# Optimization experiments

Hardware: AMD Instinct MI355X
Metric: run time of the kernel (lower is better)

## Reference

```python
import jax, jax.numpy as jnp
import numpy as np

B, LAT, NF, IMG, NC = 16, 512, 32, 128, 12
WT_FIN, WT_FOUT = NF * 64, NF                 # wave_bias_transform dyna 1x1 conv
C2C_FIN, C2C_FH, C2C_FOUT = NF * 4, NF * 2, NF * 2  # cell_to_cell dyna residual block (gated -> fout=2*NF)


def _inorm(x, eps=1e-5):
    # F.instance_norm (no affine): per-sample, per-channel over H,W
    m = x.mean(axis=(2, 3), keepdims=True)
    v = ((x - m) ** 2).mean(axis=(2, 3), keepdims=True)
    return (x - m) * jax.lax.rsqrt(v + eps)


def _sobel_kernels(nf):
    # SinSobel(nf, 3, 1): sin gradient profile x cos smoothing profile, 2 directions (c_factor=2)
    xs = jnp.array([-1.0, 0.0, 1.0], dtype=jnp.float32)
    g = jnp.sin(xs * (np.pi / 2))
    s = jnp.cos(xs * (np.pi / 2))
    ky = jnp.outer(g, s)
    kx = jnp.outer(s, g)
    k = jnp.stack([ky, kx])[:, None]          # [2,1,3,3]
    return jnp.tile(k, (nf, 1, 1, 1))         # [2*nf,1,3,3] depthwise


def _hyper(lat, w1, b1, w2, b2):
    h = jax.nn.relu(lat @ w1 + b1)
    return h @ w2 + b2


def _dyn_params(p, fin, fout, off):
    w = p[:, off:off + fin * fout].reshape(-1, fout, fin) / np.sqrt(fin)
    b = p[:, off + fin * fout: off + fin * fout + fout]
    return w, b, off + fin * fout + fout


def _econv(x, w, b):
    # per-sample dynamic 1x1 conv: x [B,I,H,W], w [B,O,I], b [B,O]
    return jnp.einsum('bihw,boi->bohw', x, w) + b[:, :, None, None]


def setup_inputs():
    key = jax.random.key(0)
    ks = jax.random.split(key, 8)
    sc = 0.02
    P = (C2C_FIN * C2C_FH + C2C_FH) + (C2C_FH * C2C_FH + C2C_FH) + \
        (C2C_FH * C2C_FOUT + C2C_FOUT) + (C2C_FIN * C2C_FOUT + C2C_FOUT)
    WP = WT_FIN * WT_FOUT + WT_FOUT
    return {
        'lat': jax.random.normal(ks[0], (B, LAT), jnp.float32),
        'leak_factor': jnp.asarray(0.1, jnp.float32),
        'wave_bias': jax.random.normal(ks[1], (1, WT_FIN, IMG, IMG), jnp.float32),
        'wt_w1': jax.random.normal(ks[2], (LAT, LAT), jnp.float32) * sc,
        'wt_b1': jnp.zeros((LAT,), jnp.float32),
        'wt_w2': jax.random.normal(ks[3], (LAT, WP), jnp.float32) * sc,
        'wt_b2': jnp.zeros((WP,), jnp.float32),
        'c2c_w1': jax.random.normal(ks[4], (LAT, 2 * LAT), jnp.float32) * sc,
        'c2c_b1': jnp.zeros((2 * LAT,), jnp.float32),
        'c2c_w2': jax.random.normal(ks[5], (2 * LAT, P), jnp.float32) * sc,
        'c2c_b2': jnp.zeros((P,), jnp.float32),
        'out_w': jax.random.normal(ks[6], (3, NF), jnp.float32) / np.sqrt(NF),
        'out_b': jnp.zeros((3,), jnp.float32),
    }


def reference(lat, leak_factor, wave_bias, wt_w1, wt_b1, wt_w2, wt_b2,
              c2c_w1, c2c_b1, c2c_w2, c2c_b2, out_w, out_b):
    b = lat.shape[0]
    # wave bias: per-sample dynamic 1x1 conv -> exp(i*x) -> cat(real, imag) -> instance norm
    pw = _hyper(lat, wt_w1, wt_b1, wt_w2, wt_b2)
    ww, wbb, _ = _dyn_params(pw, WT_FIN, WT_FOUT, 0)
    wb_flat = _econv(jnp.broadcast_to(wave_bias, (b,) + wave_bias.shape[1:]), ww, wbb)
    wave = _inorm(jnp.concatenate([jnp.cos(wb_flat), jnp.sin(wb_flat)], axis=1))  # [B,2*NF,H,W]
    leak = jnp.clip(leak_factor, 1e-3, 1e3)
    # cell_to_cell hypernetwork-generated residual-block weights (shared across calls)
    p = _hyper(lat, c2c_w1, c2c_b1, c2c_w2, c2c_b2)
    w_in, b_in, o = _dyn_params(p, C2C_FIN, C2C_FH, 0)
    w_mid, b_mid, o = _dyn_params(p, C2C_FH, C2C_FH, o)
    w_out, b_out, o = _dyn_params(p, C2C_FH, C2C_FOUT, o)
    w_sk, b_sk, o = _dyn_params(p, C2C_FIN, C2C_FOUT, o)
    kern = _sobel_kernels(NF)

    def step(out, _):
        g = _inorm(jax.lax.conv_general_dilated(
            out, kern, (1, 1), 'SAME', feature_group_count=NF,
            dimension_numbers=('NCHW', 'OIHW', 'NCHW')))
        xin = jnp.concatenate([g, wave], axis=1)             # [B,4*NF,H,W]
        h = jax.nn.leaky_relu(_econv(xin, w_in, b_in), 0.2)
        h = jax.nn.leaky_relu(_econv(h, w_mid, b_mid), 0.2)
        y = _econv(h, w_out, b_out) + _econv(xin, w_sk, b_sk)  # [B,2*NF,H,W]
        out_new = y[:, :NF] * jax.nn.sigmoid(y[:, NF:])        # gated
        nxt = out + leak * out_new
        return nxt, nxt

    out0 = jnp.zeros((b, NF, IMG, IMG), jnp.float32)
    out, embs = jax.lax.scan(step, out0, None, length=NC)
    out_embs = jnp.concatenate([out0[None], embs], axis=0)     # [NC+1,B,NF,H,W]
    out_raw = jnp.einsum('bihw,oi->bohw', out, out_w) + out_b[None, :, None, None]
    return jnp.clip(out_raw, -1.0, 1.0), out_embs, out_raw
```

## Files before the change

### kernel.cpp

```cpp
#include <hip/hip_runtime.h>
#include <hip/hip_bf16.h>
#include <stdint.h>


typedef __attribute__((ext_vector_type(8))) short s8v;
typedef __attribute__((ext_vector_type(4))) float f4v;

__device__ __forceinline__ uint16_t f2b(float f) {
    uint32_t x = __builtin_bit_cast(uint32_t, f);
    uint32_t r = (x + 0x7fffu + ((x >> 16) & 1u)) >> 16;
    return (uint16_t)r;
}

__device__ __forceinline__ float blockReduceSum(float v, float* scratch) {
    #pragma unroll
    for (int o = 32; o > 0; o >>= 1) v += __shfl_down(v, o, 64);
    int w = threadIdx.x >> 6;
    if ((threadIdx.x & 63) == 0) scratch[w] = v;
    __syncthreads();
    float r = scratch[0] + scratch[1] + scratch[2] + scratch[3];
    __syncthreads();
    return r;
}

__global__ __launch_bounds__(256) void k_hyper1(const float* __restrict__ lat,
        const float* __restrict__ w1a, const float* __restrict__ b1a,
        const float* __restrict__ w1b, const float* __restrict__ b1b,
        float* __restrict__ hwtT, float* __restrict__ hc2cT) {
    int b = blockIdx.y;
    int j = blockIdx.x * 256 + threadIdx.x;
    __shared__ float lats[512];
    for (int k = threadIdx.x; k < 512; k += 256) lats[k] = lat[b * 512 + k];
    __syncthreads();
    if (j < 512) {
        float acc = b1a[j];
        #pragma unroll 4
        for (int k = 0; k < 512; k++) acc += lats[k] * w1a[k * 512 + j];
        hwtT[j * 16 + b] = fmaxf(acc, 0.f);
    } else {
        int jj = j - 512;
        float acc = b1b[jj];
        #pragma unroll 4
        for (int k = 0; k < 512; k++) acc += lats[k] * w1b[k * 1024 + jj];
        hc2cT[jj * 16 + b] = fmaxf(acc, 0.f);
    }
}

__global__ __launch_bounds__(256) void k_hyper2(const float* __restrict__ hT,
        const float* __restrict__ w2, const float* __restrict__ b2v,
        float* __restrict__ outp, int K, int N) {
    extern __shared__ float hs[];
    for (int i = threadIdx.x; i < K * 16; i += 256) hs[i] = hT[i];
    __syncthreads();
    int col = blockIdx.x * 256 + threadIdx.x;
    if (col >= N) return;
    float acc[16];
    float bias = b2v[col];
    #pragma unroll
    for (int b = 0; b < 16; b++) acc[b] = bias;
    #pragma unroll 4
    for (int k = 0; k < K; k++) {
        float wv = w2[(size_t)k * N + col];
        const f4v* h4 = (const f4v*)(hs + k * 16);
        f4v h0 = h4[0], h1 = h4[1], h2 = h4[2], h3 = h4[3];
        acc[0]  += h0[0] * wv; acc[1]  += h0[1] * wv; acc[2]  += h0[2] * wv; acc[3]  += h0[3] * wv;
        acc[4]  += h1[0] * wv; acc[5]  += h1[1] * wv; acc[6]  += h1[2] * wv; acc[7]  += h1[3] * wv;
        acc[8]  += h2[0] * wv; acc[9]  += h2[1] * wv; acc[10] += h2[2] * wv; acc[11] += h2[3] * wv;
        acc[12] += h3[0] * wv; acc[13] += h3[1] * wv; acc[14] += h3[2] * wv; acc[15] += h3[3] * wv;
    }
    #pragma unroll
    for (int b = 0; b < 16; b++) outp[(size_t)b * N + col] = acc[b];
}

__global__ __launch_bounds__(256) void k_prepw(const float* __restrict__ pw, const float* __restrict__ pc,
        uint16_t* __restrict__ ww, uint16_t* __restrict__ wc) {
    int tid = blockIdx.x * 256 + threadIdx.x;
    const float s128 = 0.08838834764831845f;
    const float s64  = 0.125f;
    const float s2048 = 0.02209708691207961f;
    if (tid < 16 * 65536) {
        int b = tid >> 16, r = tid & 65535;
        ww[tid] = f2b(pw[(size_t)b * 65568 + r] * s2048);
    } else {
        int t = tid - 16 * 65536;
        int b = t / 24576, r = t % 24576;
        int src; float sc;
        if (r < 8192)       { src = r;                   sc = s128; }
        else if (r < 12288) { src = 8256  + (r - 8192);  sc = s64; }
        else if (r < 16384) { src = 12416 + (r - 12288); sc = s64; }
        else                { src = 16576 + (r - 16384); sc = s128; }
        wc[(size_t)b * 24576 + r] = f2b(pc[(size_t)b * 24832 + src] * sc);
    }
}

__global__ __launch_bounds__(256) void k_transpose(const float* __restrict__ wb, uint16_t* __restrict__ wbt) {
    __shared__ uint16_t tile[64][66];
    int p0 = blockIdx.x * 64, i0 = blockIdx.y * 64;
    int lane = threadIdx.x & 63, grp = threadIdx.x >> 6;
    #pragma unroll
    for (int r = 0; r < 16; r++) {
        int i = grp * 16 + r;
        tile[i][lane] = f2b(wb[(size_t)(i0 + i) * 16384 + p0 + lane]);
    }
    __syncthreads();
    #pragma unroll
    for (int r = 0; r < 16; r++) {
        int p = grp * 16 + r;
        wbt[(size_t)(p0 + p) * 2048 + i0 + lane] = tile[lane][p];
    }
}

__global__ __launch_bounds__(256) void k_wavegemm(const uint16_t* __restrict__ ww,
        const uint16_t* __restrict__ wbt, const float* __restrict__ pw, float* __restrict__ wb) {
    int nt = blockIdx.x;
    int mt = blockIdx.y;
    int w = threadIdx.x >> 6, L = threadIdx.x & 63;
    int l15 = L & 15, quad = L >> 4;
    int pxbase = nt * 256 + w * 64;
    f4v acc[4][4];
    #pragma unroll
    for (int t = 0; t < 4; t++) {
        int m = mt * 64 + t * 16 + quad * 4;
        int b = m >> 5, o = m & 31;
        f4v bv = *(const f4v*)(pw + (size_t)b * 65568 + 65536 + o);
        #pragma unroll
        for (int j = 0; j < 4; j++) acc[t][j] = bv;
    }
    for (int kk = 0; kk < 64; kk++) {
        s8v a[4], x[4];
        #pragma unroll
        for (int t = 0; t < 4; t++) {
            int m = mt * 64 + t * 16 + l15;
            a[t] = *(const s8v*)(ww + (size_t)m * 2048 + kk * 32 + quad * 8);
        }
        #pragma unroll
        for (int j = 0; j < 4; j++) {
            int p = pxbase + j * 16 + l15;
            x[j] = *(const s8v*)(wbt + (size_t)p * 2048 + kk * 32 + quad * 8);
        }
        #pragma unroll
        for (int t = 0; t < 4; t++)
            #pragma unroll
            for (int j = 0; j < 4; j++)
                acc[t][j] = __builtin_amdgcn_mfma_f32_16x16x32_bf16(a[t], x[j], acc[t][j], 0, 0, 0);
    }
    #pragma unroll
    for (int t = 0; t < 4; t++)
        #pragma unroll
        for (int j = 0; j < 4; j++)
            #pragma unroll
            for (int r = 0; r < 4; r++) {
                int row = mt * 64 + t * 16 + quad * 4 + r;
                int p = pxbase + j * 16 + l15;
                wb[(size_t)row * 16384 + p] = acc[t][j][r];
            }
}

__global__ __launch_bounds__(256) void k_wavestats(const float* __restrict__ wb, float* __restrict__ stats) {
    __shared__ float scratch[4];
    int c = blockIdx.x, b = blockIdx.y;
    const float* src = wb + (size_t)(b * 32 + (c & 31)) * 16384;
    bool isc = c < 32;
    float s = 0.f;
    for (int p = threadIdx.x; p < 16384; p += 256) {
        float x = src[p];
        s += isc ? __cosf(x) : __sinf(x);
    }
    float m = blockReduceSum(s, scratch) * (1.f / 16384.f);
    float s2 = 0.f;
    for (int p = threadIdx.x; p < 16384; p += 256) {
        float x = src[p];
        float v = (isc ? __cosf(x) : __sinf(x)) - m;
        s2 += v * v;
    }
    float tv = blockReduceSum(s2, scratch);
    if (threadIdx.x == 0) {
        stats[(b * 64 + c) * 2 + 0] = m;
        stats[(b * 64 + c) * 2 + 1] = rsqrtf(tv * (1.f / 16384.f) + 1e-5f);
    }
}

__global__ __launch_bounds__(256) void k_wavewrite(const float* __restrict__ wb,
        const float* __restrict__ stats, uint16_t* __restrict__ xin) {
    __shared__ uint16_t tl[256][66];
    int b = blockIdx.y, p0 = blockIdx.x * 256;
    int t = threadIdx.x;
    for (int c = 0; c < 64; c++) {
        int row = b * 32 + (c & 31);
        float m  = stats[(b * 64 + c) * 2 + 0];
        float rs = stats[(b * 64 + c) * 2 + 1];
        float x = wb[(size_t)row * 16384 + p0 + t];
        float v = (c < 32) ? __cosf(x) : __sinf(x);
        tl[t][c] = f2b((v - m) * rs);
    }
    __syncthreads();
    uint16_t* dst = xin + ((size_t)(b * 16384 + p0 + t) * 128 + 64);
    const uint32_t* s32 = (const uint32_t*)&tl[t][0];
    #pragma unroll
    for (int c8 = 0; c8 < 64; c8 += 8) {
        uint4 v;
        v.x = s32[c8 / 2 + 0]; v.y = s32[c8 / 2 + 1];
        v.z = s32[c8 / 2 + 2]; v.w = s32[c8 / 2 + 3];
        *(uint4*)(dst + c8) = v;
    }
}

__global__ __launch_bounds__(256) void k_gstats(const float* __restrict__ outs, float* __restrict__ stats) {
    __shared__ float scratch[4];
    int ic = blockIdx.x, b = blockIdx.y;
    const float* src = outs + (size_t)(b * 32 + ic) * 16384;
    float sy = 0.f, sy2 = 0.f, sx = 0.f, sx2 = 0.f;
    for (int p = threadIdx.x; p < 16384; p += 256) {
        int y = p >> 7, x = p & 127;
        float up = (y > 0)   ? src[p - 128] : 0.f;
        float dn = (y < 127) ? src[p + 128] : 0.f;
        float lf = (x > 0)   ? src[p - 1]   : 0.f;
        float rt = (x < 127) ? src[p + 1]   : 0.f;
        float vy = dn - up, vx = rt - lf;
        sy += vy; sy2 += vy * vy; sx += vx; sx2 += vx * vx;
    }
    float SY  = blockReduceSum(sy,  scratch);
    float SY2 = blockReduceSum(sy2, scratch);
    float SX  = blockReduceSum(sx,  scratch);
    float SX2 = blockReduceSum(sx2, scratch);
    if (threadIdx.x == 0) {
        float my = SY * (1.f / 16384.f);
        float vy = fmaxf(SY2 * (1.f / 16384.f) - my * my, 0.f);
        float mx = SX * (1.f / 16384.f);
        float vx = fmaxf(SX2 * (1.f / 16384.f) - mx * mx, 0.f);
        stats[(b * 64 + 2 * ic) * 2 + 0] = my;
        stats[(b * 64 + 2 * ic) * 2 + 1] = rsqrtf(vy + 1e-5f);
        stats[(b * 64 + 2 * ic + 1) * 2 + 0] = mx;
        stats[(b * 64 + 2 * ic + 1) * 2 + 1] = rsqrtf(vx + 1e-5f);
    }
}

__global__ __launch_bounds__(256) void k_gwrite(const float* __restrict__ outs,
        const float* __restrict__ stats, uint16_t* __restrict__ xin) {
    __shared__ uint16_t tl[256][66];
    int b = blockIdx.y, p0 = blockIdx.x * 256;
    int t = threadIdx.x;
    int p = p0 + t;
    int y = p >> 7, x = p & 127;
    for (int ic = 0; ic < 32; ic++) {
        const float* src = outs + (size_t)(b * 32 + ic) * 16384;
        float up = (y > 0)   ? src[p - 128] : 0.f;
        float dn = (y < 127) ? src[p + 128] : 0.f;
        float lf = (x > 0)   ? src[p - 1]   : 0.f;
        float rt = (x < 127) ? src[p + 1]   : 0.f;
        int o = 2 * ic;
        float m0 = stats[(b * 64 + o) * 2], r0 = stats[(b * 64 + o) * 2 + 1];
        float m1 = stats[(b * 64 + o + 1) * 2], r1 = stats[(b * 64 + o + 1) * 2 + 1];
        tl[t][o]     = f2b((dn - up - m0) * r0);
        tl[t][o + 1] = f2b((rt - lf - m1) * r1);
    }
    __syncthreads();
    uint16_t* dst = xin + (size_t)(b * 16384 + p) * 128;
    const uint32_t* s32 = (const uint32_t*)&tl[t][0];
    #pragma unroll
    for (int c8 = 0; c8 < 64; c8 += 8) {
        uint4 v;
        v.x = s32[c8 / 2 + 0]; v.y = s32[c8 / 2 + 1];
        v.z = s32[c8 / 2 + 2]; v.w = s32[c8 / 2 + 3];
        *(uint4*)(dst + c8) = v;
    }
}

__global__ __launch_bounds__(256) void k_conv(const uint16_t* __restrict__ wc,
        const uint16_t* __restrict__ xin, const float* __restrict__ pc,
        float* __restrict__ outs, float* __restrict__ embs, const float* __restrict__ leakp) {
    __shared__ uint16_t Hs[256][72];
    int b = blockIdx.y, p0 = blockIdx.x * 256;
    int w = threadIdx.x >> 6, L = threadIdx.x & 63;
    int l15 = L & 15, quad = L >> 4;
    const uint16_t* wcb = wc + (size_t)b * 24576;
    const float* pcb = pc + (size_t)b * 24832;
    size_t xbase = ((size_t)b * 16384 + p0 + w * 64) * 128;

    f4v acc[4][4];
    #pragma unroll
    for (int t = 0; t < 4; t++) {
        f4v bv = *(const f4v*)(pcb + 8192 + t * 16 + quad * 4);
        #pragma unroll
        for (int j = 0; j < 4; j++) acc[t][j] = bv;
    }
    #pragma unroll
    for (int kk = 0; kk < 4; kk++) {
        s8v a[4], x[4];
        #pragma unroll
        for (int t = 0; t < 4; t++)
            a[t] = *(const s8v*)(wcb + (size_t)(t * 16 + l15) * 128 + kk * 32 + quad * 8);
        #pragma unroll
        for (int j = 0; j < 4; j++)
            x[j] = *(const s8v*)(xin + xbase + (size_t)(j * 16 + l15) * 128 + kk * 32 + quad * 8);
        #pragma unroll
        for (int t = 0; t < 4; t++)
            #pragma unroll
            for (int j = 0; j < 4; j++)
                acc[t][j] = __builtin_amdgcn_mfma_f32_16x16x32_bf16(a[t], x[j], acc[t][j], 0, 0, 0);
    }
    #pragma unroll
    for (int t = 0; t < 4; t++)
        #pragma unroll
        for (int j = 0; j < 4; j++) {
            uint16_t pk[4];
            #pragma unroll
            for (int r = 0; r < 4; r++) {
                float v = acc[t][j][r];
                pk[r] = f2b(v > 0.f ? v : 0.2f * v);
            }
            int px = w * 64 + j * 16 + l15;
            int ch = t * 16 + quad * 4;
            uint2 u; u.x = (uint32_t)pk[0] | ((uint32_t)pk[1] << 16);
            u.y = (uint32_t)pk[2] | ((uint32_t)pk[3] << 16);
            *(uint2*)&Hs[px][ch] = u;
        }
    __syncthreads();

    f4v acc2[4][4];
    #pragma unroll
    for (int t = 0; t < 4; t++) {
        f4v bv = *(const f4v*)(pcb + 12352 + t * 16 + quad * 4);
        #pragma unroll
        for (int j = 0; j < 4; j++) acc2[t][j] = bv;
    }
    #pragma unroll
    for (int kk = 0; kk < 2; kk++) {
        s8v a[4], h[4];
        #pragma unroll
        for (int t = 0; t < 4; t++)
            a[t] = *(const s8v*)(wcb + 8192 + (size_t)(t * 16 + l15) * 64 + kk * 32 + quad * 8);
        #pragma unroll
        for (int j = 0; j < 4; j++) {
            int px = w * 64 + j * 16 + l15;
            h[j] = *(const s8v*)&Hs[px][kk * 32 + quad * 8];
        }
        #pragma unroll
        for (int t = 0; t < 4; t++)
            #pragma unroll
            for (int j = 0; j < 4; j++)
                acc2[t][j] = __builtin_amdgcn_mfma_f32_16x16x32_bf16(a[t], h[j], acc2[t][j], 0, 0, 0);
    }
    __syncthreads();
    #pragma unroll
    for (int t = 0; t < 4; t++)
        #pragma unroll
        for (int j = 0; j < 4; j++) {
            uint16_t pk[4];
            #pragma unroll
            for (int r = 0; r < 4; r++) {
                float v = acc2[t][j][r];
                pk[r] = f2b(v > 0.f ? v : 0.2f * v);
            }
            int px = w * 64 + j * 16 + l15;
            int ch = t * 16 + quad * 4;
            uint2 u; u.x = (uint32_t)pk[0] | ((uint32_t)pk[1] << 16);
            u.y = (uint32_t)pk[2] | ((uint32_t)pk[3] << 16);
            *(uint2*)&Hs[px][ch] = u;
        }
    __syncthreads();

    f4v acc3[4][4];
    #pragma unroll
    for (int t = 0; t < 4; t++) {
        f4v b1 = *(const f4v*)(pcb + 16512 + t * 16 + quad * 4);
        f4v b2 = *(const f4v*)(pcb + 24768 + t * 16 + quad * 4);
        f4v bv = b1 + b2;
        #pragma unroll
        for (int j = 0; j < 4; j++) acc3[t][j] = bv;
    }
    #pragma unroll
    for (int kk = 0; kk < 2; kk++) {
        s8v a[4], h[4];
        #pragma unroll
        for (int t = 0; t < 4; t++)
            a[t] = *(const s8v*)(wcb + 12288 + (size_t)(t * 16 + l15) * 64 + kk * 32 + quad * 8);
        #pragma unroll
        for (int j = 0; j < 4; j++) {
            int px = w * 64 + j * 16 + l15;
            h[j] = *(const s8v*)&Hs[px][kk * 32 + quad * 8];
        }
        #pragma unroll
        for (int t = 0; t < 4; t++)
            #pragma unroll
            for (int j = 0; j < 4; j++)
                acc3[t][j] = __builtin_amdgcn_mfma_f32_16x16x32_bf16(a[t], h[j], acc3[t][j], 0, 0, 0);
    }
    #pragma unroll
    for (int kk = 0; kk < 4; kk++) {
        s8v a[4], x[4];
        #pragma unroll
        for (int t = 0; t < 4; t++)
            a[t] = *(const s8v*)(wcb + 16384 + (size_t)(t * 16 + l15) * 128 + kk * 32 + quad * 8);
        #pragma unroll
        for (int j = 0; j < 4; j++)
            x[j] = *(const s8v*)(xin + xbase + (size_t)(j * 16 + l15) * 128 + kk * 32 + quad * 8);
        #pragma unroll
        for (int t = 0; t < 4; t++)
            #pragma unroll
            for (int j = 0; j < 4; j++)
                acc3[t][j] = __builtin_amdgcn_mfma_f32_16x16x32_bf16(a[t], x[j], acc3[t][j], 0, 0, 0);
    }

    float leak = leakp[0];
    leak = fminf(fmaxf(leak, 0.001f), 1000.f);
    #pragma unroll
    for (int t = 0; t < 2; t++)
        #pragma unroll
        for (int j = 0; j < 4; j++) {
            int px = p0 + w * 64 + j * 16 + l15;
            #pragma unroll
            for (int r = 0; r < 4; r++) {
                int ch = t * 16 + quad * 4 + r;
                float y1 = acc3[t][j][r];
                float y2 = acc3[t + 2][j][r];
                float on = y1 / (1.f + __expf(-y2));
                size_t idx = (size_t)(b * 32 + ch) * 16384 + px;
                float nx = outs[idx] + leak * on;
                outs[idx] = nx;
                embs[idx] = nx;
            }
        }
}

__global__ __launch_bounds__(256) void k_final(const float* __restrict__ outs,
        const float* __restrict__ ow, const float* __restrict__ ob,
        float* __restrict__ dclip, float* __restrict__ draw) {
    __shared__ float ws[3][32];
    __shared__ float obs[3];
    int b = blockIdx.y, p0 = blockIdx.x * 256;
    int t = threadIdx.x;
    if (t < 96) ws[t / 32][t % 32] = ow[t];
    if (t < 3) obs[t] = ob[t];
    __syncthreads();
    int p = p0 + t;
    float a0 = obs[0], a1 = obs[1], a2 = obs[2];
    #pragma unroll 4
    for (int c = 0; c < 32; c++) {
        float v = outs[(size_t)(b * 32 + c) * 16384 + p];
        a0 += v * ws[0][c]; a1 += v * ws[1][c]; a2 += v * ws[2][c];
    }
    float raw[3] = {a0, a1, a2};
    #pragma unroll
    for (int oc = 0; oc < 3; oc++) {
        size_t idx = (size_t)(b * 3 + oc) * 16384 + p;
        draw[idx] = raw[oc];
        dclip[idx] = fminf(fmaxf(raw[oc], -1.f), 1.f);
    }
}

extern "C" void kernel_launch(void* const* d_in, const int* in_sizes, int n_in,
                              void* d_out, int out_size, void* d_ws, size_t ws_size,
                              hipStream_t stream) {
    const float* lat   = (const float*)d_in[0];
    const float* leakp = (const float*)d_in[1];
    const float* wbias = (const float*)d_in[2];
    const float* wtw1  = (const float*)d_in[3];
    const float* wtb1  = (const float*)d_in[4];
    const float* wtw2  = (const float*)d_in[5];
    const float* wtb2  = (const float*)d_in[6];
    const float* cw1   = (const float*)d_in[7];
    const float* cb1   = (const float*)d_in[8];
    const float* cw2   = (const float*)d_in[9];
    const float* cb2   = (const float*)d_in[10];
    const float* outw  = (const float*)d_in[11];
    const float* outb  = (const float*)d_in[12];
    float* out_f = (float*)d_out;

    char* ws = (char*)d_ws;
    float*    hwtT  = (float*)(ws + 0);
    float*    hc2cT = (float*)(ws + 32768);
    float*    pw    = (float*)(ws + 98304);
    float*    pc    = (float*)(ws + 4294656);
    uint16_t* ww    = (uint16_t*)(ws + 5883904);
    uint16_t* wc    = (uint16_t*)(ws + 7981056);
    float*    statw = (float*)(ws + 8767488);
    float*    statg = (float*)(ws + 8775680);
    float*    wb    = (float*)(ws + 8783872);
    uint16_t* wbt   = (uint16_t*)(ws + 42338304);
    uint16_t* xin   = (uint16_t*)(ws + 109447168);
    float*    outs  = (float*)(ws + 176556032);

    hipMemsetAsync(outs, 0, 33554432, stream);
    hipMemsetAsync(out_f + 786432, 0, 33554432, stream);

    k_hyper1<<<dim3(6, 16), 256, 0, stream>>>(lat, wtw1, wtb1, cw1, cb1, hwtT, hc2cT);
    k_hyper2<<<dim3(257), 256, 32768, stream>>>(hwtT, wtw2, wtb2, pw, 512, 65568);
    k_hyper2<<<dim3(97), 256, 65536, stream>>>(hc2cT, cw2, cb2, pc, 1024, 24832);
    k_prepw<<<dim3(5632), 256, 0, stream>>>(pw, pc, ww, wc);
    k_transpose<<<dim3(256, 32), 256, 0, stream>>>(wbias, wbt);
    k_wavegemm<<<dim3(64, 8), 256, 0, stream>>>(ww, wbt, pw, wb);
    k_wavestats<<<dim3(64, 16), 256, 0, stream>>>(wb, statw);
    k_wavewrite<<<dim3(64, 16), 256, 0, stream>>>(wb, statw, xin);

    for (int it = 0; it < 12; ++it) {
        k_gstats<<<dim3(32, 16), 256, 0, stream>>>(outs, statg);
        k_gwrite<<<dim3(64, 16), 256, 0, stream>>>(outs, statg, xin);
        k_conv<<<dim3(64, 16), 256, 0, stream>>>(wc, xin, pc, outs,
                out_f + 786432 + (size_t)(it + 1) * 8388608, leakp);
    }
    k_final<<<dim3(64, 16), 256, 0, stream>>>(outs, outw, outb, out_f, out_f + 109838336);
}
```

Measured before the change: 2.466 ms.

## Ping-pong state through embedding slots, fuse sin/cos stats, remap wave GEMM blocks

The recurrent state is no longer kept in a separate buffer. Each step reads the previous embedding slot and writes the next one, which removes a read-modify-write and a duplicate store per step, and the first gstats launch is skipped because it would read an all-zero state. The wave stats kernel now computes the cos and sin statistics in one pass over half as many blocks, and wavewrite computes sincos once per element with the stats cached in shared memory. The wave GEMM gets an XCD-aware block-to-tile mapping plus a 2x unroll, and the conv kernel computes the skip GEMM together with the first GEMM so the x loads are shared, at the cost of higher register pressure from holding two accumulator sets.

```diff
diff --git a/kernel.cpp b/kernel.cpp
--- a/kernel.cpp
+++ b/kernel.cpp
@@ -112,8 +112,10 @@
 
 __global__ __launch_bounds__(256) void k_wavegemm(const uint16_t* __restrict__ ww,
         const uint16_t* __restrict__ wbt, const float* __restrict__ pw, float* __restrict__ wb) {
-    int nt = blockIdx.x;
-    int mt = blockIdx.y;
+    int id = blockIdx.x;
+    int xcd = id & 7, slot = id >> 3;
+    int nt = xcd * 8 + (slot >> 3);
+    int mt = slot & 7;
     int w = threadIdx.x >> 6, L = threadIdx.x & 63;
     int l15 = L & 15, quad = L >> 4;
     int pxbase = nt * 256 + w * 64;
@@ -126,6 +128,7 @@
         #pragma unroll
         for (int j = 0; j < 4; j++) acc[t][j] = bv;
     }
+    #pragma unroll 2
     for (int kk = 0; kk < 64; kk++) {
         s8v a[4], x[4];
         #pragma unroll
@@ -159,39 +162,43 @@
 __global__ __launch_bounds__(256) void k_wavestats(const float* __restrict__ wb, float* __restrict__ stats) {
     __shared__ float scratch[4];
     int c = blockIdx.x, b = blockIdx.y;
-    const float* src = wb + (size_t)(b * 32 + (c & 31)) * 16384;
-    bool isc = c < 32;
-    float s = 0.f;
+    const float* src = wb + (size_t)(b * 32 + c) * 16384;
+    float sc = 0.f, sc2 = 0.f, ss = 0.f, ss2 = 0.f;
     for (int p = threadIdx.x; p < 16384; p += 256) {
         float x = src[p];
-        s += isc ? __cosf(x) : __sinf(x);
-    }
-    float m = blockReduceSum(s, scratch) * (1.f / 16384.f);
-    float s2 = 0.f;
-    for (int p = threadIdx.x; p < 16384; p += 256) {
-        float x = src[p];
-        float v = (isc ? __cosf(x) : __sinf(x)) - m;
-        s2 += v * v;
-    }
-    float tv = blockReduceSum(s2, scratch);
+        float cv = __cosf(x), sv = __sinf(x);
+        sc += cv; sc2 += cv * cv; ss += sv; ss2 += sv * sv;
+    }
+    float SC  = blockReduceSum(sc,  scratch);
+    float SC2 = blockReduceSum(sc2, scratch);
+    float SS  = blockReduceSum(ss,  scratch);
+    float SS2 = blockReduceSum(ss2, scratch);
     if (threadIdx.x == 0) {
-        stats[(b * 64 + c) * 2 + 0] = m;
-        stats[(b * 64 + c) * 2 + 1] = rsqrtf(tv * (1.f / 16384.f) + 1e-5f);
+        float mc = SC * (1.f / 16384.f);
+        float vc = fmaxf(SC2 * (1.f / 16384.f) - mc * mc, 0.f);
+        float ms = SS * (1.f / 16384.f);
+        float vs = fmaxf(SS2 * (1.f / 16384.f) - ms * ms, 0.f);
+        stats[(b * 64 + c) * 2 + 0] = mc;
+        stats[(b * 64 + c) * 2 + 1] = rsqrtf(vc + 1e-5f);
+        stats[(b * 64 + 32 + c) * 2 + 0] = ms;
+        stats[(b * 64 + 32 + c) * 2 + 1] = rsqrtf(vs + 1e-5f);
     }
 }
 
 __global__ __launch_bounds__(256) void k_wavewrite(const float* __restrict__ wb,
         const float* __restrict__ stats, uint16_t* __restrict__ xin) {
     __shared__ uint16_t tl[256][66];
+    __shared__ float sst[128];
     int b = blockIdx.y, p0 = blockIdx.x * 256;
     int t = threadIdx.x;
-    for (int c = 0; c < 64; c++) {
-        int row = b * 32 + (c & 31);
-        float m  = stats[(b * 64 + c) * 2 + 0];
-        float rs = stats[(b * 64 + c) * 2 + 1];
+    if (t < 128) sst[t] = stats[b * 128 + t];
+    __syncthreads();
+    for (int c = 0; c < 32; c++) {
+        int row = b * 32 + c;
         float x = wb[(size_t)row * 16384 + p0 + t];
-        float v = (c < 32) ? __cosf(x) : __sinf(x);
-        tl[t][c] = f2b((v - m) * rs);
+        float cv = __cosf(x), sv = __sinf(x);
+        tl[t][c]      = f2b((cv - sst[2 * c]) * sst[2 * c + 1]);
+        tl[t][c + 32] = f2b((sv - sst[64 + 2 * c]) * sst[64 + 2 * c + 1]);
     }
     __syncthreads();
     uint16_t* dst = xin + ((size_t)(b * 16384 + p0 + t) * 128 + 64);
@@ -205,10 +212,10 @@
     }
 }
 
-__global__ __launch_bounds__(256) void k_gstats(const float* __restrict__ outs, float* __restrict__ stats) {
+__global__ __launch_bounds__(256) void k_gstats(const float* __restrict__ prev, float* __restrict__ stats) {
     __shared__ float scratch[4];
     int ic = blockIdx.x, b = blockIdx.y;
-    const float* src = outs + (size_t)(b * 32 + ic) * 16384;
+    const float* src = prev + (size_t)(b * 32 + ic) * 16384;
     float sy = 0.f, sy2 = 0.f, sx = 0.f, sx2 = 0.f;
     for (int p = threadIdx.x; p < 16384; p += 256) {
         int y = p >> 7, x = p & 127;
@@ -235,7 +242,7 @@
     }
 }
 
-__global__ __launch_bounds__(256) void k_gwrite(const float* __restrict__ outs,
+__global__ __launch_bounds__(256) void k_gwrite(const float* __restrict__ prev,
         const float* __restrict__ stats, uint16_t* __restrict__ xin) {
     __shared__ uint16_t tl[256][66];
     int b = blockIdx.y, p0 = blockIdx.x * 256;
@@ -243,7 +250,7 @@
     int p = p0 + t;
     int y = p >> 7, x = p & 127;
     for (int ic = 0; ic < 32; ic++) {
-        const float* src = outs + (size_t)(b * 32 + ic) * 16384;
+        const float* src = prev + (size_t)(b * 32 + ic) * 16384;
         float up = (y > 0)   ? src[p - 128] : 0.f;
         float dn = (y < 127) ? src[p + 128] : 0.f;
         float lf = (x > 0)   ? src[p - 1]   : 0.f;
@@ -268,7 +275,8 @@
 
 __global__ __launch_bounds__(256) void k_conv(const uint16_t* __restrict__ wc,
         const uint16_t* __restrict__ xin, const float* __restrict__ pc,
-        float* __restrict__ outs, float* __restrict__ embs, const float* __restrict__ leakp) {
+        const float* __restrict__ prev, float* __restrict__ next,
+        const float* __restrict__ leakp) {
     __shared__ uint16_t Hs[256][72];
     int b = blockIdx.y, p0 = blockIdx.x * 256;
     int w = threadIdx.x >> 6, L = threadIdx.x & 63;
@@ -277,27 +285,36 @@
     const float* pcb = pc + (size_t)b * 24832;
     size_t xbase = ((size_t)b * 16384 + p0 + w * 64) * 128;
 
-    f4v acc[4][4];
+    f4v acc1[4][4], acc3[4][4];
     #pragma unroll
     for (int t = 0; t < 4; t++) {
-        f4v bv = *(const f4v*)(pcb + 8192 + t * 16 + quad * 4);
-        #pragma unroll
-        for (int j = 0; j < 4; j++) acc[t][j] = bv;
+        f4v bv1 = *(const f4v*)(pcb + 8192 + t * 16 + quad * 4);
+        f4v bo  = *(const f4v*)(pcb + 16512 + t * 16 + quad * 4);
+        f4v bs  = *(const f4v*)(pcb + 24768 + t * 16 + quad * 4);
+        f4v bv3 = bo + bs;
+        #pragma unroll
+        for (int j = 0; j < 4; j++) { acc1[t][j] = bv1; acc3[t][j] = bv3; }
     }
     #pragma unroll
     for (int kk = 0; kk < 4; kk++) {
-        s8v a[4], x[4];
-        #pragma unroll
-        for (int t = 0; t < 4; t++)
-            a[t] = *(const s8v*)(wcb + (size_t)(t * 16 + l15) * 128 + kk * 32 + quad * 8);
+        s8v x[4];
         #pragma unroll
         for (int j = 0; j < 4; j++)
             x[j] = *(const s8v*)(xin + xbase + (size_t)(j * 16 + l15) * 128 + kk * 32 + quad * 8);
         #pragma unroll
-        for (int t = 0; t < 4; t++)
+        for (int t = 0; t < 4; t++) {
+            s8v a1 = *(const s8v*)(wcb + (size_t)(t * 16 + l15) * 128 + kk * 32 + quad * 8);
             #pragma unroll
             for (int j = 0; j < 4; j++)
-                acc[t][j] = __builtin_amdgcn_mfma_f32_16x16x32_bf16(a[t], x[j], acc[t][j], 0, 0, 0);
+                acc1[t][j] = __builtin_amdgcn_mfma_f32_16x16x32_bf16(a1, x[j], acc1[t][j], 0, 0, 0);
+        }
+        #pragma unroll
+        for (int t = 0; t < 4; t++) {
+            s8v a3 = *(const s8v*)(wcb + 16384 + (size_t)(t * 16 + l15) * 128 + kk * 32 + quad * 8);
+            #pragma unroll
+            for (int j = 0; j < 4; j++)
+                acc3[t][j] = __builtin_amdgcn_mfma_f32_16x16x32_bf16(a3, x[j], acc3[t][j], 0, 0, 0);
+        }
     }
     #pragma unroll
     for (int t = 0; t < 4; t++)
@@ -306,7 +323,7 @@
             uint16_t pk[4];
             #pragma unroll
             for (int r = 0; r < 4; r++) {
-                float v = acc[t][j][r];
+                float v = acc1[t][j][r];
                 pk[r] = f2b(v > 0.f ? v : 0.2f * v);
             }
             int px = w * 64 + j * 16 + l15;
@@ -360,15 +377,6 @@
         }
     __syncthreads();
 
-    f4v acc3[4][4];
-    #pragma unroll
-    for (int t = 0; t < 4; t++) {
-        f4v b1 = *(const f4v*)(pcb + 16512 + t * 16 + quad * 4);
-        f4v b2 = *(const f4v*)(pcb + 24768 + t * 16 + quad * 4);
-        f4v bv = b1 + b2;
-        #pragma unroll
-        for (int j = 0; j < 4; j++) acc3[t][j] = bv;
-    }
     #pragma unroll
     for (int kk = 0; kk < 2; kk++) {
         s8v a[4], h[4];
@@ -385,21 +393,6 @@
             #pragma unroll
             for (int j = 0; j < 4; j++)
                 acc3[t][j] = __builtin_amdgcn_mfma_f32_16x16x32_bf16(a[t], h[j], acc3[t][j], 0, 0, 0);
-    }
-    #pragma unroll
-    for (int kk = 0; kk < 4; kk++) {
-        s8v a[4], x[4];
-        #pragma unroll
-        for (int t = 0; t < 4; t++)
-            a[t] = *(const s8v*)(wcb + 16384 + (size_t)(t * 16 + l15) * 128 + kk * 32 + quad * 8);
-        #pragma unroll
-        for (int j = 0; j < 4; j++)
-            x[j] = *(const s8v*)(xin + xbase + (size_t)(j * 16 + l15) * 128 + kk * 32 + quad * 8);
-        #pragma unroll
-        for (int t = 0; t < 4; t++)
-            #pragma unroll
-            for (int j = 0; j < 4; j++)
-                acc3[t][j] = __builtin_amdgcn_mfma_f32_16x16x32_bf16(a[t], x[j], acc3[t][j], 0, 0, 0);
     }
 
     float leak = leakp[0];
@@ -416,9 +409,7 @@
                 float y2 = acc3[t + 2][j][r];
                 float on = y1 / (1.f + __expf(-y2));
                 size_t idx = (size_t)(b * 32 + ch) * 16384 + px;
-                float nx = outs[idx] + leak * on;
-                outs[idx] = nx;
-                embs[idx] = nx;
+                next[idx] = prev[idx] + leak * on;
             }
         }
 }
@@ -479,25 +470,29 @@
     float*    wb    = (float*)(ws + 8783872);
     uint16_t* wbt   = (uint16_t*)(ws + 42338304);
     uint16_t* xin   = (uint16_t*)(ws + 109447168);
-    float*    outs  = (float*)(ws + 176556032);
-
-    hipMemsetAsync(outs, 0, 33554432, stream);
-    hipMemsetAsync(out_f + 786432, 0, 33554432, stream);
+
+    float* emb0 = out_f + 786432;
+
+    hipMemsetAsync(emb0, 0, 33554432, stream);
+    hipMemsetAsync(statg, 0, 8192, stream);
 
     k_hyper1<<<dim3(6, 16), 256, 0, stream>>>(lat, wtw1, wtb1, cw1, cb1, hwtT, hc2cT);
     k_hyper2<<<dim3(257), 256, 32768, stream>>>(hwtT, wtw2, wtb2, pw, 512, 65568);
     k_hyper2<<<dim3(97), 256, 65536, stream>>>(hc2cT, cw2, cb2, pc, 1024, 24832);
     k_prepw<<<dim3(5632), 256, 0, stream>>>(pw, pc, ww, wc);
     k_transpose<<<dim3(256, 32), 256, 0, stream>>>(wbias, wbt);
-    k_wavegemm<<<dim3(64, 8), 256, 0, stream>>>(ww, wbt, pw, wb);
-    k_wavestats<<<dim3(64, 16), 256, 0, stream>>>(wb, statw);
+    k_wavegemm<<<dim3(512), 256, 0, stream>>>(ww, wbt, pw, wb);
+    k_wavestats<<<dim3(32, 16), 256, 0, stream>>>(wb, statw);
     k_wavewrite<<<dim3(64, 16), 256, 0, stream>>>(wb, statw, xin);
 
     for (int it = 0; it < 12; ++it) {
-        k_gstats<<<dim3(32, 16), 256, 0, stream>>>(outs, statg);
-        k_gwrite<<<dim3(64, 16), 256, 0, stream>>>(outs, statg, xin);
-        k_conv<<<dim3(64, 16), 256, 0, stream>>>(wc, xin, pc, outs,
-                out_f + 786432 + (size_t)(it + 1) * 8388608, leakp);
-    }
-    k_final<<<dim3(64, 16), 256, 0, stream>>>(outs, outw, outb, out_f, out_f + 109838336);
-}
+        const float* prev = emb0 + (size_t)it * 8388608;
+        float* next = emb0 + (size_t)(it + 1) * 8388608;
+        if (it > 0)
+            k_gstats<<<dim3(32, 16), 256, 0, stream>>>(prev, statg);
+        k_gwrite<<<dim3(64, 16), 256, 0, stream>>>(prev, statg, xin);
+        k_conv<<<dim3(64, 16), 256, 0, stream>>>(wc, xin, pc, prev, next, leakp);
+    }
+    k_final<<<dim3(64, 16), 256, 0, stream>>>(emb0 + (size_t)12 * 8388608, outw, outb,
+                                              out_f, out_f + 109838336);
+}
```

New measurement: 2.331 ms. 1.06x faster.
